# Optimization experiments

Hardware: AMD Instinct MI355X
Metric: run time of the kernel (lower is better)

The kernel has to match this reference:

```python
import jax, jax.numpy as jnp
import numpy as np

N, F, H, C = 8192, 512, 1, 128   # nodes, in-features, heads, channels
NEG_SLOPE = 0.2
EDGE_P = 0.004                    # ~33 avg degree


def setup_inputs() -> dict:
    key = jax.random.key(0)
    k1, k2, k3, k4, k5 = jax.random.split(key, 5)
    features = jax.random.normal(k1, (N, F), dtype=jnp.float32)
    # binary adjacency (dense materialization of the tf.sparse adjacency)
    adjacency = (jax.random.uniform(k2, (N, N)) < EDGE_P).astype(jnp.float32)
    # learned params (glorot-ish scale)
    kernel = jax.random.normal(k3, (F, H * C), dtype=jnp.float32) * 0.05
    att_src = jax.random.normal(k4, (1, H, C), dtype=jnp.float32) * 0.05
    att_dst = jax.random.normal(k5, (1, H, C), dtype=jnp.float32) * 0.05
    return {"features": features, "adjacency": adjacency,
            "kernel": kernel, "att_src": att_src, "att_dst": att_dst}


def reference(features, adjacency, kernel, att_src, att_dst):
    ft = features @ kernel                      # (N, H*C)
    ft3 = ft.reshape(-1, H, C)                  # (N, H, C)
    a_src = jnp.sum(ft3 * att_src, axis=-1)     # (N, H) -> (N, 1) since H==1
    a_dst = jnp.sum(ft3 * att_dst, axis=-1)     # (N, 1)
    scores = a_src + a_dst.T                    # (N, N) via broadcast (H==1)
    # sparse multiply + to_dense == dense elementwise mask with binary adjacency
    masked = scores * adjacency                 # (N, N)
    masked = jnp.where(masked >= 0, masked, NEG_SLOPE * masked)  # leaky_relu
    coeff = jax.nn.softmax(masked, axis=-1)     # dense row softmax (incl. zeros)
    # dropout_rate == 0.0 -> identity
    out = coeff @ ft                            # (N, H*C)
    return jax.nn.elu(out)
```

## Files before the change

kernel.cpp:

```cpp
#include <hip/hip_runtime.h>
#include <hip/hip_bf16.h>
#include <hip/hip_fp16.h>
#include <math.h>

#define N_NODES 8192
#define F_IN    512
#define C_OUT   128
#define CSR_CAP 128
#define NEG_SLOPE 0.2f

typedef float f4v __attribute__((ext_vector_type(4)));

__device__ __forceinline__ int lane_lt_popc(unsigned long long m) {
  return __builtin_amdgcn_mbcnt_hi((unsigned)(m >> 32),
         __builtin_amdgcn_mbcnt_lo((unsigned)m, 0u));
}

__global__ void __launch_bounds__(512, 8) fat_kernel(
    const float* __restrict__ adj, int* __restrict__ counts,
    unsigned short* __restrict__ elist,
    const float* __restrict__ X, const float* __restrict__ W,
    const float* __restrict__ att_src, const float* __restrict__ att_dst,
    __half* __restrict__ ft16, float* __restrict__ asrc,
    float* __restrict__ adst, float* __restrict__ Spart)
{
  __shared__ float sx[32][36];
  __shared__ float sk[32][132];

  const int bid = blockIdx.x;
  const int tid = threadIdx.x;

  if (bid < 256) {
    const int row0 = bid * 32;
    const int rg   = tid >> 6;
    const int r0   = rg * 4;
    const int lane = tid & 63;
    const int c0   = lane * 2;

    float acc[4][2] = {};

    for (int kt = 0; kt < F_IN; kt += 32) {
      if (tid < 256) {
        int row = tid >> 3, kv = (tid & 7) * 4;
        f4v v = *(const f4v*)(X + (size_t)(row0 + row) * F_IN + kt + kv);
        *(f4v*)&sx[row][kv] = v;
      }
      #pragma unroll
      for (int q = 0; q < 2; ++q) {
        int idx = q * 512 + tid;
        int kk  = idx >> 5;
        int cc  = (idx & 31) * 4;
        *(f4v*)&sk[kk][cc] = *(const f4v*)(W + (size_t)(kt + kk) * C_OUT + cc);
      }
      __syncthreads();
      #pragma unroll 4
      for (int k = 0; k < 32; ++k) {
        float2 b = *(const float2*)&sk[k][c0];
        #pragma unroll
        for (int i = 0; i < 4; ++i) {
          float a = sx[r0 + i][k];
          acc[i][0] += a * b.x;
          acc[i][1] += a * b.y;
        }
      }
      __syncthreads();
    }

    #pragma unroll
    for (int i = 0; i < 4; ++i) {
      __half2 h = __floats2half2_rn(acc[i][0], acc[i][1]);
      ((__half2*)ft16)[(size_t)(row0 + r0 + i) * 64 + lane] = h;
    }

    float2 as = *(const float2*)(att_src + c0);
    float2 ad = *(const float2*)(att_dst + c0);
    #pragma unroll
    for (int i = 0; i < 4; ++i) {
      float ps = acc[i][0] * as.x + acc[i][1] * as.y;
      float pd = acc[i][0] * ad.x + acc[i][1] * ad.y;
      #pragma unroll
      for (int off = 32; off > 0; off >>= 1) {
        ps += __shfl_xor(ps, off);
        pd += __shfl_xor(pd, off);
      }
      if (lane == 0) {
        asrc[row0 + r0 + i] = ps;
        adst[row0 + r0 + i] = pd;
      }
    }

    float* scp = &sx[0][0];
    float s0 = acc[0][0] + acc[1][0] + acc[2][0] + acc[3][0];
    float s1 = acc[0][1] + acc[1][1] + acc[2][1] + acc[3][1];
    *(float2*)&scp[rg * 128 + c0] = make_float2(s0, s1);
    __syncthreads();
    if (tid < 128) {
      float s = 0.f;
      #pragma unroll
      for (int q = 0; q < 8; ++q) s += scp[q * 128 + tid];
      Spart[(size_t)bid * 128 + tid] = s;
    }
  } else {
    const int sb   = bid - 256;
    const int lane = tid & 63;
    const int wv   = tid >> 6;
    const int row  = sb * 8 + wv;
    const f4v* rp  = (const f4v*)(adj + (size_t)row * N_NODES);
    unsigned short* er = elist + (size_t)row * CSR_CAP;

    int base = 0;
    for (int cb = 0; cb < 32; cb += 8) {
      f4v v[8];
      #pragma unroll
      for (int q = 0; q < 8; ++q)
        v[q] = __builtin_nontemporal_load(&rp[(cb + q) * 64 + lane]);
      #pragma unroll
      for (int q = 0; q < 8; ++q) {
        const int colb = (cb + q) * 256 + lane * 4;
        unsigned long long b0 = __ballot(v[q][0] != 0.f);
        unsigned long long b1 = __ballot(v[q][1] != 0.f);
        unsigned long long b2 = __ballot(v[q][2] != 0.f);
        unsigned long long b3 = __ballot(v[q][3] != 0.f);
        int o = base + lane_lt_popc(b0) + lane_lt_popc(b1)
                     + lane_lt_popc(b2) + lane_lt_popc(b3);
        if ((b0 >> lane) & 1ull) { if (o < CSR_CAP) er[o] = (unsigned short)(colb + 0); ++o; }
        if ((b1 >> lane) & 1ull) { if (o < CSR_CAP) er[o] = (unsigned short)(colb + 1); ++o; }
        if ((b2 >> lane) & 1ull) { if (o < CSR_CAP) er[o] = (unsigned short)(colb + 2); ++o; }
        if ((b3 >> lane) & 1ull) { if (o < CSR_CAP) er[o] = (unsigned short)(colb + 3); ++o; }
        base += __popcll(b0) + __popcll(b1) + __popcll(b2) + __popcll(b3);
      }
    }
    if (lane == 0) counts[row] = base < CSR_CAP ? base : CSR_CAP;
  }
}

__global__ void __launch_bounds__(256) colsum_par_kernel(
    const float* __restrict__ Spart, float* __restrict__ S)
{
  __shared__ float wpart[4];
  const int c = blockIdx.x;
  const int t = threadIdx.x;
  const int lane = t & 63, w = t >> 6;
  float v = Spart[(size_t)t * 128 + c];
  #pragma unroll
  for (int off = 32; off > 0; off >>= 1) v += __shfl_xor(v, off);
  if (lane == 0) wpart[w] = v;
  __syncthreads();
  if (t == 0) S[c] = wpart[0] + wpart[1] + wpart[2] + wpart[3];
}

__global__ void __launch_bounds__(512) gather_all_kernel(
    const int* __restrict__ counts, const unsigned short* __restrict__ elist,
    const __half* __restrict__ ft16, const float* __restrict__ asrc,
    const float* __restrict__ adst, const float* __restrict__ S,
    float* __restrict__ out)
{
  __shared__ int   sj[8][CSR_CAP];
  __shared__ float sw[8][CSR_CAP];

  const int lane = threadIdx.x & 63;
  const int wv   = threadIdx.x >> 6;
  const int row  = blockIdx.x * 8 + wv;
  const int cnt  = counts[row];
  const float ai = asrc[row];
  const unsigned short* er = elist + (size_t)row * CSR_CAP;

  float dsum = 0.f;
  for (int e = lane; e < cnt; e += 64) {
    int j = er[e];
    float s = ai + adst[j];
    float l = s < 0.f ? NEG_SLOPE * s : s;
    float w = expf(l);
    sj[wv][e] = j;
    sw[wv][e] = w - 1.0f;
    dsum += w;
  }
  #pragma unroll
  for (int off = 32; off > 0; off >>= 1) dsum += __shfl_xor(dsum, off);
  const float denom = (float)(N_NODES - cnt) + dsum;

  float2 acc = make_float2(0.f, 0.f);
  const __half2* f2 = (const __half2*)ft16;
  int e = 0;
  for (; e + 8 <= cnt; e += 8) {
    int   j0 = sj[wv][e+0], j1 = sj[wv][e+1], j2 = sj[wv][e+2], j3 = sj[wv][e+3];
    int   j4 = sj[wv][e+4], j5 = sj[wv][e+5], j6 = sj[wv][e+6], j7 = sj[wv][e+7];
    float2 f0 = __half22float2(f2[(size_t)j0 * 64 + lane]);
    float2 f1 = __half22float2(f2[(size_t)j1 * 64 + lane]);
    float2 g2 = __half22float2(f2[(size_t)j2 * 64 + lane]);
    float2 f3 = __half22float2(f2[(size_t)j3 * 64 + lane]);
    float2 f4 = __half22float2(f2[(size_t)j4 * 64 + lane]);
    float2 f5 = __half22float2(f2[(size_t)j5 * 64 + lane]);
    float2 f6 = __half22float2(f2[(size_t)j6 * 64 + lane]);
    float2 f7 = __half22float2(f2[(size_t)j7 * 64 + lane]);
    float w0 = sw[wv][e+0], w1 = sw[wv][e+1], w2 = sw[wv][e+2], w3 = sw[wv][e+3];
    float w4 = sw[wv][e+4], w5 = sw[wv][e+5], w6 = sw[wv][e+6], w7 = sw[wv][e+7];
    acc.x += w0 * f0.x; acc.y += w0 * f0.y;
    acc.x += w1 * f1.x; acc.y += w1 * f1.y;
    acc.x += w2 * g2.x; acc.y += w2 * g2.y;
    acc.x += w3 * f3.x; acc.y += w3 * f3.y;
    acc.x += w4 * f4.x; acc.y += w4 * f4.y;
    acc.x += w5 * f5.x; acc.y += w5 * f5.y;
    acc.x += w6 * f6.x; acc.y += w6 * f6.y;
    acc.x += w7 * f7.x; acc.y += w7 * f7.y;
  }
  for (; e < cnt; ++e) {
    int   j = sj[wv][e];
    float w = sw[wv][e];
    float2 f = __half22float2(f2[(size_t)j * 64 + lane]);
    acc.x += w * f.x; acc.y += w * f.y;
  }

  float2 sv = ((const float2*)S)[lane];
  float ox = (sv.x + acc.x) / denom;
  float oy = (sv.y + acc.y) / denom;
  ox = ox > 0.f ? ox : expm1f(ox);
  oy = oy > 0.f ? oy : expm1f(oy);
  ((float2*)out)[(size_t)row * 64 + lane] = make_float2(ox, oy);
}

extern "C" void kernel_launch(void* const* d_in, const int* in_sizes, int n_in,
                              void* d_out, int out_size, void* d_ws, size_t ws_size,
                              hipStream_t stream)
{
  const float* X       = (const float*)d_in[0];
  const float* adj     = (const float*)d_in[1];
  const float* W       = (const float*)d_in[2];
  const float* att_src = (const float*)d_in[3];
  const float* att_dst = (const float*)d_in[4];
  float* out = (float*)d_out;

  float* ws    = (float*)d_ws;
  float* asrc  = ws;
  float* adst  = asrc + N_NODES;
  float* Spart = adst + N_NODES;
  float* S     = Spart + 256 * 128;
  int*   counts = (int*)(S + 128);
  __half* ft16 = (__half*)(counts + N_NODES);
  unsigned short* elist =
      (unsigned short*)(ft16 + (size_t)N_NODES * C_OUT);

  fat_kernel<<<1280, 512, 0, stream>>>(adj, counts, elist,
                                       X, W, att_src, att_dst,
                                       ft16, asrc, adst, Spart);
  colsum_par_kernel<<<128, 256, 0, stream>>>(Spart, S);
  gather_all_kernel<<<N_NODES / 8, 512, 0, stream>>>(counts, elist, ft16,
                                                     asrc, adst, S, out);
}
```

Measured before the change: 68.10 us.

## Use fp16 MFMA for feature projection and precompute attention vectors

Adds a prep kernel that transposes W into fp16 and folds att_src/att_dst into per-input-feature vectors u=W·a_src and v=W·a_dst. The main projection then runs on 16x16x32 f16 MFMA instructions instead of scalar FMAs, and the attention scores come straight from X·u and X·v in fp32. This cuts ALU time in the GEMM part of the fused kernel but adds an extra launch and lowers the GEMM input precision to fp16.

```diff
diff --git a/kernel.cpp b/kernel.cpp
--- a/kernel.cpp
+++ b/kernel.cpp
@@ -9,97 +9,123 @@
 #define CSR_CAP 128
 #define NEG_SLOPE 0.2f
 
-typedef float f4v __attribute__((ext_vector_type(4)));
+typedef float f4v  __attribute__((ext_vector_type(4)));
+typedef float f32x4 __attribute__((ext_vector_type(4)));
+typedef _Float16 f16x8 __attribute__((ext_vector_type(8)));
 
 __device__ __forceinline__ int lane_lt_popc(unsigned long long m) {
   return __builtin_amdgcn_mbcnt_hi((unsigned)(m >> 32),
          __builtin_amdgcn_mbcnt_lo((unsigned)m, 0u));
 }
 
-__global__ void __launch_bounds__(512, 8) fat_kernel(
+__global__ void __launch_bounds__(512) prep_kernel(
+    const float* __restrict__ W, const float* __restrict__ att_src,
+    const float* __restrict__ att_dst, float* __restrict__ u,
+    float* __restrict__ v, _Float16* __restrict__ wT16)
+{
+  const int lane = threadIdx.x & 63;
+  const int w    = threadIdx.x >> 6;
+  const int k    = blockIdx.x * 8 + w;
+  float2 wv = *(const float2*)(W + (size_t)k * C_OUT + lane * 2);
+  float2 a1 = *(const float2*)(att_src + lane * 2);
+  float2 a2 = *(const float2*)(att_dst + lane * 2);
+  float pu = wv.x * a1.x + wv.y * a1.y;
+  float pv = wv.x * a2.x + wv.y * a2.y;
+  wT16[(size_t)(lane * 2 + 0) * F_IN + k] = (_Float16)wv.x;
+  wT16[(size_t)(lane * 2 + 1) * F_IN + k] = (_Float16)wv.y;
+  #pragma unroll
+  for (int off = 32; off > 0; off >>= 1) {
+    pu += __shfl_xor(pu, off);
+    pv += __shfl_xor(pv, off);
+  }
+  if (lane == 0) { u[k] = pu; v[k] = pv; }
+}
+
+__global__ void __launch_bounds__(512) fat_kernel(
     const float* __restrict__ adj, int* __restrict__ counts,
     unsigned short* __restrict__ elist,
-    const float* __restrict__ X, const float* __restrict__ W,
-    const float* __restrict__ att_src, const float* __restrict__ att_dst,
-    __half* __restrict__ ft16, float* __restrict__ asrc,
+    const float* __restrict__ X, const _Float16* __restrict__ wT16,
+    const float* __restrict__ u, const float* __restrict__ v,
+    _Float16* __restrict__ ft16, float* __restrict__ asrc,
     float* __restrict__ adst, float* __restrict__ Spart)
 {
-  __shared__ float sx[32][36];
-  __shared__ float sk[32][132];
+  __shared__ _Float16 axb[32][72];
+  __shared__ _Float16 wkb[128][72];
 
   const int bid = blockIdx.x;
   const int tid = threadIdx.x;
 
   if (bid < 256) {
+    const int lane = tid & 63;
+    const int wv_  = tid >> 6;
+    const int rt   = wv_ >> 2;
+    const int ct0  = (wv_ & 3) * 2;
     const int row0 = bid * 32;
-    const int rg   = tid >> 6;
-    const int r0   = rg * 4;
-    const int lane = tid & 63;
-    const int c0   = lane * 2;
-
-    float acc[4][2] = {};
-
-    for (int kt = 0; kt < F_IN; kt += 32) {
-      if (tid < 256) {
-        int row = tid >> 3, kv = (tid & 7) * 4;
-        f4v v = *(const f4v*)(X + (size_t)(row0 + row) * F_IN + kt + kv);
-        *(f4v*)&sx[row][kv] = v;
-      }
+    const int srow = tid >> 4;
+    const int sk4  = (tid & 15) * 4;
+
+    f32x4 D0 = {0.f, 0.f, 0.f, 0.f};
+    f32x4 D1 = {0.f, 0.f, 0.f, 0.f};
+    float pa = 0.f, pd = 0.f;
+
+    for (int kt = 0; kt < F_IN; kt += 64) {
+      f4v xv = *(const f4v*)(X + (size_t)(row0 + srow) * F_IN + kt + sk4);
+      f4v u4 = *(const f4v*)(u + kt + sk4);
+      f4v w4 = *(const f4v*)(v + kt + sk4);
+      pa += xv[0]*u4[0] + xv[1]*u4[1] + xv[2]*u4[2] + xv[3]*u4[3];
+      pd += xv[0]*w4[0] + xv[1]*w4[1] + xv[2]*w4[2] + xv[3]*w4[3];
+      axb[srow][sk4 + 0] = (_Float16)xv[0];
+      axb[srow][sk4 + 1] = (_Float16)xv[1];
+      axb[srow][sk4 + 2] = (_Float16)xv[2];
+      axb[srow][sk4 + 3] = (_Float16)xv[3];
       #pragma unroll
       for (int q = 0; q < 2; ++q) {
         int idx = q * 512 + tid;
-        int kk  = idx >> 5;
-        int cc  = (idx & 31) * 4;
-        *(f4v*)&sk[kk][cc] = *(const f4v*)(W + (size_t)(kt + kk) * C_OUT + cc);
+        int c   = idx >> 3;
+        int k8  = (idx & 7) * 8;
+        *(f16x8*)&wkb[c][k8] = *(const f16x8*)(wT16 + (size_t)c * F_IN + kt + k8);
       }
       __syncthreads();
-      #pragma unroll 4
-      for (int k = 0; k < 32; ++k) {
-        float2 b = *(const float2*)&sk[k][c0];
-        #pragma unroll
-        for (int i = 0; i < 4; ++i) {
-          float a = sx[r0 + i][k];
-          acc[i][0] += a * b.x;
-          acc[i][1] += a * b.y;
-        }
+      #pragma unroll
+      for (int s = 0; s < 2; ++s) {
+        f16x8 a  = *(const f16x8*)&axb[rt * 16 + (lane & 15)][s * 32 + (lane >> 4) * 8];
+        f16x8 b0 = *(const f16x8*)&wkb[ct0 * 16 + (lane & 15)][s * 32 + (lane >> 4) * 8];
+        f16x8 b1 = *(const f16x8*)&wkb[(ct0 + 1) * 16 + (lane & 15)][s * 32 + (lane >> 4) * 8];
+        D0 = __builtin_amdgcn_mfma_f32_16x16x32_f16(a, b0, D0, 0, 0, 0);
+        D1 = __builtin_amdgcn_mfma_f32_16x16x32_f16(a, b1, D1, 0, 0, 0);
       }
       __syncthreads();
     }
 
     #pragma unroll
-    for (int i = 0; i < 4; ++i) {
-      __half2 h = __floats2half2_rn(acc[i][0], acc[i][1]);
-      ((__half2*)ft16)[(size_t)(row0 + r0 + i) * 64 + lane] = h;
-    }
-
-    float2 as = *(const float2*)(att_src + c0);
-    float2 ad = *(const float2*)(att_dst + c0);
+    for (int reg = 0; reg < 4; ++reg) {
+      int r = row0 + rt * 16 + (lane >> 4) * 4 + reg;
+      ft16[(size_t)r * C_OUT + ct0 * 16 + (lane & 15)]       = (_Float16)D0[reg];
+      ft16[(size_t)r * C_OUT + (ct0 + 1) * 16 + (lane & 15)] = (_Float16)D1[reg];
+    }
+
     #pragma unroll
-    for (int i = 0; i < 4; ++i) {
-      float ps = acc[i][0] * as.x + acc[i][1] * as.y;
-      float pd = acc[i][0] * ad.x + acc[i][1] * ad.y;
-      #pragma unroll
-      for (int off = 32; off > 0; off >>= 1) {
-        ps += __shfl_xor(ps, off);
-        pd += __shfl_xor(pd, off);
-      }
-      if (lane == 0) {
-        asrc[row0 + r0 + i] = ps;
-        adst[row0 + r0 + i] = pd;
-      }
-    }
-
-    float* scp = &sx[0][0];
-    float s0 = acc[0][0] + acc[1][0] + acc[2][0] + acc[3][0];
-    float s1 = acc[0][1] + acc[1][1] + acc[2][1] + acc[3][1];
-    *(float2*)&scp[rg * 128 + c0] = make_float2(s0, s1);
+    for (int off = 8; off > 0; off >>= 1) {
+      pa += __shfl_xor(pa, off);
+      pd += __shfl_xor(pd, off);
+    }
+    if ((tid & 15) == 0) {
+      asrc[row0 + srow] = pa;
+      adst[row0 + srow] = pd;
+    }
+
+    float cs0 = D0[0] + D0[1] + D0[2] + D0[3];
+    float cs1 = D1[0] + D1[1] + D1[2] + D1[3];
+    cs0 += __shfl_xor(cs0, 16); cs0 += __shfl_xor(cs0, 32);
+    cs1 += __shfl_xor(cs1, 16); cs1 += __shfl_xor(cs1, 32);
+    float* sp = (float*)&axb[0][0];
+    if (lane < 16) {
+      sp[rt * 128 + ct0 * 16 + lane]      = cs0;
+      sp[rt * 128 + ct0 * 16 + 16 + lane] = cs1;
+    }
     __syncthreads();
-    if (tid < 128) {
-      float s = 0.f;
-      #pragma unroll
-      for (int q = 0; q < 8; ++q) s += scp[q * 128 + tid];
-      Spart[(size_t)bid * 128 + tid] = s;
-    }
+    if (tid < 128)
+      Spart[(size_t)bid * 128 + tid] = sp[tid] + sp[128 + tid];
   } else {
     const int sb   = bid - 256;
     const int lane = tid & 63;
@@ -110,17 +136,17 @@
 
     int base = 0;
     for (int cb = 0; cb < 32; cb += 8) {
-      f4v v[8];
+      f4v vv[8];
       #pragma unroll
       for (int q = 0; q < 8; ++q)
-        v[q] = __builtin_nontemporal_load(&rp[(cb + q) * 64 + lane]);
+        vv[q] = __builtin_nontemporal_load(&rp[(cb + q) * 64 + lane]);
       #pragma unroll
       for (int q = 0; q < 8; ++q) {
         const int colb = (cb + q) * 256 + lane * 4;
-        unsigned long long b0 = __ballot(v[q][0] != 0.f);
-        unsigned long long b1 = __ballot(v[q][1] != 0.f);
-        unsigned long long b2 = __ballot(v[q][2] != 0.f);
-        unsigned long long b3 = __ballot(v[q][3] != 0.f);
+        unsigned long long b0 = __ballot(vv[q][0] != 0.f);
+        unsigned long long b1 = __ballot(vv[q][1] != 0.f);
+        unsigned long long b2 = __ballot(vv[q][2] != 0.f);
+        unsigned long long b3 = __ballot(vv[q][3] != 0.f);
         int o = base + lane_lt_popc(b0) + lane_lt_popc(b1)
                      + lane_lt_popc(b2) + lane_lt_popc(b3);
         if ((b0 >> lane) & 1ull) { if (o < CSR_CAP) er[o] = (unsigned short)(colb + 0); ++o; }
@@ -235,15 +261,21 @@
   float* adst  = asrc + N_NODES;
   float* Spart = adst + N_NODES;
   float* S     = Spart + 256 * 128;
-  int*   counts = (int*)(S + 128);
-  __half* ft16 = (__half*)(counts + N_NODES);
+  float* u     = S + 128;
+  float* v     = u + 512;
+  int*   counts = (int*)(v + 512);
+  _Float16* ft16 = (_Float16*)(counts + N_NODES);
   unsigned short* elist =
       (unsigned short*)(ft16 + (size_t)N_NODES * C_OUT);
-
+  _Float16* wT16 =
+      (_Float16*)(elist + (size_t)N_NODES * CSR_CAP);
+
+  prep_kernel<<<64, 512, 0, stream>>>(W, att_src, att_dst, u, v, wT16);
   fat_kernel<<<1280, 512, 0, stream>>>(adj, counts, elist,
-                                       X, W, att_src, att_dst,
+                                       X, wT16, u, v,
                                        ft16, asrc, adst, Spart);
   colsum_par_kernel<<<128, 256, 0, stream>>>(Spart, S);
-  gather_all_kernel<<<N_NODES / 8, 512, 0, stream>>>(counts, elist, ft16,
+  gather_all_kernel<<<N_NODES / 8, 512, 0, stream>>>(counts, elist,
+                                                     (const __half*)ft16,
                                                      asrc, adst, S, out);
 }
```

Result: slower. 71.27 us (+4.6%).
